# Optimization experiments

Hardware: AMD Instinct MI355X
Metric: run time of the kernel (lower is better)

The kernel has to match this reference:

```python
import jax, jax.numpy as jnp
import numpy as np

HIDDEN = 256
HEADS = 8
HEAD_DIM = HIDDEN // HEADS
RBF_DIM = 50
EPS = 1e-5


def setup_inputs() -> dict:
    key = jax.random.key(0)
    ks = jax.random.split(key, 16)
    L, P = 1024, 2048
    s = 0.02
    inp = {
        "lig_h": jax.random.normal(ks[0], (L, HIDDEN), jnp.float32),
        "prot_h": jax.random.normal(ks[1], (P, HIDDEN), jnp.float32),
        "rbf": jax.random.uniform(ks[2], (L, P, RBF_DIM), jnp.float32),
        "L": L,
        "P": P,
        "Wq": jax.random.normal(ks[3], (HIDDEN, HIDDEN), jnp.float32) * s,
        "bq": jnp.zeros((HIDDEN,), jnp.float32),
        "Wk": jax.random.normal(ks[4], (HIDDEN, HIDDEN), jnp.float32) * s,
        "bk": jnp.zeros((HIDDEN,), jnp.float32),
        "Wv": jax.random.normal(ks[5], (HIDDEN, HIDDEN), jnp.float32) * s,
        "bv": jnp.zeros((HIDDEN,), jnp.float32),
        "Wrbf": jax.random.normal(ks[6], (RBF_DIM, HEADS), jnp.float32) * s,
        "brbf": jnp.zeros((HEADS,), jnp.float32),
        "Wo": jax.random.normal(ks[7], (HIDDEN, HIDDEN), jnp.float32) * s,
        "bo": jnp.zeros((HIDDEN,), jnp.float32),
        "gamma": jnp.ones((HIDDEN,), jnp.float32),
        "beta": jnp.zeros((HIDDEN,), jnp.float32),
    }
    return inp


def reference(lig_h, prot_h, rbf, L, P, Wq, bq, Wk, bk, Wv, bv, Wrbf, brbf, Wo, bo, gamma, beta):
    scale = float(HEAD_DIM) ** 0.5
    Q = (lig_h @ Wq + bq).reshape(L, HEADS, HEAD_DIM)
    K = (prot_h @ Wk + bk).reshape(P, HEADS, HEAD_DIM)
    V = (prot_h @ Wv + bv).reshape(P, HEADS, HEAD_DIM)
    attn = jnp.einsum('lhd,phd->lph', Q, K) / scale
    dist_bias = rbf @ Wrbf + brbf          # [L, P, H]
    attn = attn + dist_bias
    attn_weights = jax.nn.softmax(attn, axis=1)  # over P (protein) axis
    attended = jnp.einsum('lph,phd->lhd', attn_weights, V).reshape(L, HIDDEN)
    y = lig_h + attended @ Wo + bo
    mu = jnp.mean(y, axis=-1, keepdims=True)
    var = jnp.var(y, axis=-1, keepdims=True)
    lig_h_out = (y - mu) * jax.lax.rsqrt(var + EPS) * gamma + beta
    return (lig_h_out, attn_weights)
```

## Files before the change

kernel.cpp:

```cpp
#include <hip/hip_runtime.h>
#include <hip/hip_bf16.h>

#define L_SZ 1024
#define P_SZ 2048
#define HID 256
#define NH 8
#define HD 32
#define NRBF 50
#define CH 32
#define NCH 64

typedef unsigned int uint32;
typedef _Float16 half2_t __attribute__((ext_vector_type(2)));
typedef __fp16 fp16x2_t __attribute__((ext_vector_type(2)));

__constant__ float kINV_SCALE = 0.17677669529663687f;

static __device__ __forceinline__ unsigned short f2h(float f) {
    union { _Float16 h; unsigned short u; } x; x.h = (_Float16)f; return x.u;
}
static __device__ __forceinline__ float h2f(unsigned short u) {
    union { unsigned short u; _Float16 h; } x; x.u = u; return (float)x.h;
}
static __device__ __forceinline__ half2_t u2h2(uint32 u) {
    union { uint32 u; half2_t h; } x; x.u = u; return x.h;
}
static __device__ __forceinline__ half2_t pk2h(float a, float b) {
    union { fp16x2_t p; half2_t h; } x; x.p = __builtin_amdgcn_cvt_pkrtz(a, b); return x.h;
}

static __device__ __forceinline__ void g2l16(const void* g, void* l) {
    __builtin_amdgcn_global_load_lds(
        (__attribute__((address_space(1))) void*)(void*)g,
        (__attribute__((address_space(3))) void*)l, 16, 0, 0);
}
static __device__ __forceinline__ void g2l4(const void* g, void* l) {
    __builtin_amdgcn_global_load_lds(
        (__attribute__((address_space(1))) void*)(void*)g,
        (__attribute__((address_space(3))) void*)l, 4, 0, 0);
}

__global__ __launch_bounds__(64) void k_proj(
    const float* __restrict__ lig, const float* __restrict__ prot,
    const float* __restrict__ Wq, const float* __restrict__ bq,
    const float* __restrict__ Wk, const float* __restrict__ bk,
    const float* __restrict__ Wv, const float* __restrict__ bv,
    float* __restrict__ Qf, unsigned short* __restrict__ Kb,
    unsigned short* __restrict__ Vb)
{
    __shared__ float As[8 * HID];
    const int t = threadIdx.x;
    const int r0 = blockIdx.x * 8;

    const float* src; const float* W; const float* bias; int mode; int row0;
    if (r0 < L_SZ)            { src = lig  + (size_t)r0 * HID;               W = Wq; bias = bq; mode = 0; row0 = r0; }
    else if (r0 < L_SZ + P_SZ){ src = prot + (size_t)(r0 - L_SZ) * HID;      W = Wk; bias = bk; mode = 1; row0 = r0 - L_SZ; }
    else                      { src = prot + (size_t)(r0 - L_SZ - P_SZ)*HID; W = Wv; bias = bv; mode = 2; row0 = r0 - L_SZ - P_SZ; }

    float4* A4 = (float4*)As;
    const float4* S4 = (const float4*)src;
    #pragma unroll
    for (int j = 0; j < 8; ++j) A4[t + j * 64] = S4[t + j * 64];
    __syncthreads();

    float acc[8][4];
    #pragma unroll
    for (int r = 0; r < 8; ++r)
        #pragma unroll
        for (int c = 0; c < 4; ++c) acc[r][c] = 0.f;

    for (int k4 = 0; k4 < 64; ++k4) {
        float4 av[8];
        #pragma unroll
        for (int r = 0; r < 8; ++r) av[r] = A4[r * 64 + k4];
        #pragma unroll
        for (int kk = 0; kk < 4; ++kk) {
            const float* wr = W + (size_t)(k4 * 4 + kk) * HID + t;
            #pragma unroll
            for (int c = 0; c < 4; ++c) {
                float wv = wr[c * 64];
                #pragma unroll
                for (int r = 0; r < 8; ++r)
                    acc[r][c] += ((const float*)&av[r])[kk] * wv;
            }
        }
    }

    #pragma unroll
    for (int c = 0; c < 4; ++c) {
        const int col = t + c * 64;
        const float bb = bias[col];
        #pragma unroll
        for (int r = 0; r < 8; ++r) {
            float v = acc[r][c] + bb;
            size_t idx = (size_t)(row0 + r) * HID + col;
            if (mode == 0)      Qf[idx] = v;
            else if (mode == 1) Kb[idx] = f2h(v);
            else                Vb[idx] = f2h(v);
        }
    }
}

__global__ __launch_bounds__(256, 2) void k_attn(
    const float* __restrict__ rbf, const float* __restrict__ Qf,
    const unsigned short* __restrict__ Kb, const unsigned short* __restrict__ Vb,
    const float* __restrict__ Wrbf, const float* __restrict__ brbf,
    float* __restrict__ attn_out, float* __restrict__ att_ws)
{
    __shared__ __align__(16) char sm[78400];
    char* slgB = sm + 45568;
    float* red = (float*)(sm + 78336);

    const int t = threadIdx.x;
    const int lane = t & 63;
    const int wv = t >> 6;
    const int r = t & 31;
    const int h = t >> 5;
    const int l = blockIdx.x;

    auto stageKV = [&](const unsigned short* src, int c, char* dst) {
        const char* gb = (const char*)src + (size_t)c * (CH * 512);
        #pragma unroll
        for (int k = 0; k < 4; ++k) {
            int s = wv * 4 + k;
            int row = s * 2 + (lane >> 5);
            int off = ((lane & 31) ^ (row & 31)) << 4;
            g2l16(gb + row * 512 + off, dst + s * 1024);
        }
    };
    auto stageRBF = [&](int c, char* dst) {
        const char* gb = (const char*)rbf + (size_t)l * 409600 + (size_t)c * 6400;
        g2l16(gb + wv * 1024 + (lane << 4), dst + wv * 1024);
        if (wv == 0)      g2l16(gb + 4096 + (lane << 4), dst + 4096);
        else if (wv == 1) g2l16(gb + 5120 + (lane << 4), dst + 5120);
        else if (wv == 2) g2l4 (gb + 6144 + (lane << 2), dst + 6144);
    };

    half2_t wrb[25];
    #pragma unroll
    for (int j = 0; j < 25; ++j)
        wrb[j] = pk2h(Wrbf[(2 * j) * NH + h], Wrbf[(2 * j + 1) * NH + h]);
    const float bh = brbf[h];

    half2_t qp[16];
    {
        const float* qq = Qf + (size_t)l * HID + h * HD;
        #pragma unroll
        for (int n = 0; n < 16; ++n)
            qp[n] = pk2h(qq[2 * n], qq[2 * n + 1]);
    }

    const int doff = ((((h >> 1) ^ ((r >> 3) & 3)) << 2) | ((h & 1) << 1));

    stageKV(Kb, 0, sm);
    stageRBF(0, sm + 32768);
    asm volatile("s_waitcnt vmcnt(0)" ::: "memory");
    __syncthreads();

    float mx = -3.0e38f;
    for (int c = 0; c < NCH; ++c) {
        const int cb = c & 1;
        char* kb = sm + cb * 16384;
        char* rb = sm + 32768 + cb * 6400;
        if (c + 1 < NCH) {
            stageKV(Kb, c + 1, sm + (cb ^ 1) * 16384);
            stageRBF(c + 1, sm + 32768 + (cb ^ 1) * 6400);
        }
        float bias = bh;
        const char* rrow = rb + r * 200;
        #pragma unroll
        for (int j = 0; j < 25; ++j) {
            float2 v = *(const float2*)(rrow + j * 8);
            bias = __builtin_amdgcn_fdot2(pk2h(v.x, v.y), wrb[j], bias, false);
        }
        float qk = 0.f;
        const char* krow = kb + r * 512;
        #pragma unroll
        for (int jw = 0; jw < 4; ++jw) {
            int off = (h * 64 + jw * 16) ^ (r << 4);
            uint4 kk = *(const uint4*)(krow + off);
            qk = __builtin_amdgcn_fdot2(u2h2(kk.x), qp[jw * 4 + 0], qk, false);
            qk = __builtin_amdgcn_fdot2(u2h2(kk.y), qp[jw * 4 + 1], qk, false);
            qk = __builtin_amdgcn_fdot2(u2h2(kk.z), qp[jw * 4 + 2], qk, false);
            qk = __builtin_amdgcn_fdot2(u2h2(kk.w), qp[jw * 4 + 3], qk, false);
        }
        float lg = qk * kINV_SCALE + bias;
        mx = fmaxf(mx, lg);
        *(unsigned short*)(slgB + (size_t)((c * CH + r) * 16) + doff) = f2h(lg);

        asm volatile("s_waitcnt vmcnt(0)" ::: "memory");
        __syncthreads();
    }

    #pragma unroll
    for (int msk = 1; msk <= 16; msk <<= 1) mx = fmaxf(mx, __shfl_xor(mx, msk));
    float sme = 0.f;
    for (int c = 0; c < NCH; ++c) {
        unsigned short u = *(const unsigned short*)(slgB + (size_t)((c * CH + r) * 16) + doff);
        sme += __expf(h2f(u) - mx);
    }
    #pragma unroll
    for (int msk = 1; msk <= 16; msk <<= 1) sme += __shfl_xor(sme, msk);
    if ((t & 31) == 0) { red[h * 2] = mx; red[h * 2 + 1] = 1.f / sme; }

    stageKV(Vb, 0, sm);
    __syncthreads();

    {
        float mh[8], ih[8];
        #pragma unroll
        for (int hh = 0; hh < 8; ++hh) { mh[hh] = red[hh * 2]; ih[hh] = red[hh * 2 + 1]; }
        const int sel = t & 1;
        float m0 = sel ? mh[4] : mh[0], i0 = sel ? ih[4] : ih[0];
        float m1 = sel ? mh[5] : mh[1], i1 = sel ? ih[5] : ih[1];
        float m2 = sel ? mh[6] : mh[2], i2 = sel ? ih[6] : ih[2];
        float m3 = sel ? mh[7] : mh[3], i3 = sel ? ih[7] : ih[3];
        const int x = (t >> 4) & 3;
        const int dA = (((2 * sel)     ^ x) << 2);
        const int dB = (((2 * sel + 1) ^ x) << 2);
        float4* ao = (float4*)(attn_out + (size_t)l * (P_SZ * NH));
        #pragma unroll
        for (int n = 0; n < 16; ++n) {
            int f = t + n * 256;
            int p = (t >> 1) + n * 128;
            char* rowp = slgB + p * 16;
            uint32 a = *(uint32*)(rowp + dA);
            uint32 b = *(uint32*)(rowp + dB);
            float w0 = __expf(h2f((unsigned short)(a & 0xffffu)) - m0) * i0;
            float w1 = __expf(h2f((unsigned short)(a >> 16))     - m1) * i1;
            float w2 = __expf(h2f((unsigned short)(b & 0xffffu)) - m2) * i2;
            float w3 = __expf(h2f((unsigned short)(b >> 16))     - m3) * i3;
            ao[f] = make_float4(w0, w1, w2, w3);
            *(uint32*)(rowp + dA) = (uint32)f2h(w0) | ((uint32)f2h(w1) << 16);
            *(uint32*)(rowp + dB) = (uint32)f2h(w2) | ((uint32)f2h(w3) << 16);
        }
    }
    asm volatile("s_waitcnt vmcnt(0)" ::: "memory");
    __syncthreads();

    {
        const int h3 = t >> 5;
        const int dq = (t >> 3) & 3;
        const int ps = t & 7;
        const int vinner = h3 * 64 + dq * 16;
        float acc[8] = {0.f, 0.f, 0.f, 0.f, 0.f, 0.f, 0.f, 0.f};
        for (int c = 0; c < NCH; ++c) {
            const int cb = c & 1;
            char* vb = sm + cb * 16384;
            if (c + 1 < NCH) stageKV(Vb, c + 1, sm + (cb ^ 1) * 16384);
            #pragma unroll
            for (int m = 0; m < 4; ++m) {
                int rr = m * 8 + ps;
                int p = c * CH + rr;
                int dw = (((h3 >> 1) ^ m) << 2) | ((h3 & 1) << 1);
                float w = h2f(*(const unsigned short*)(slgB + p * 16 + dw));
                int off = vinner ^ (rr << 4);
                uint4 vvv = *(const uint4*)(vb + rr * 512 + off);
                half2_t x0 = u2h2(vvv.x), x1 = u2h2(vvv.y), x2 = u2h2(vvv.z), x3 = u2h2(vvv.w);
                acc[0] += w * (float)x0.x; acc[1] += w * (float)x0.y;
                acc[2] += w * (float)x1.x; acc[3] += w * (float)x1.y;
                acc[4] += w * (float)x2.x; acc[5] += w * (float)x2.y;
                acc[6] += w * (float)x3.x; acc[7] += w * (float)x3.y;
            }
            asm volatile("s_waitcnt vmcnt(0)" ::: "memory");
            __syncthreads();
        }
        #pragma unroll
        for (int d = 0; d < 8; ++d) {
            acc[d] += __shfl_xor(acc[d], 1);
            acc[d] += __shfl_xor(acc[d], 2);
            acc[d] += __shfl_xor(acc[d], 4);
        }
        if (ps == 0) {
            float* dst = att_ws + (size_t)l * HID + h3 * HD + dq * 8;
            *(float4*)dst       = make_float4(acc[0], acc[1], acc[2], acc[3]);
            *(float4*)(dst + 4) = make_float4(acc[4], acc[5], acc[6], acc[7]);
        }
    }
}

__global__ __launch_bounds__(256) void k_out(
    const float* __restrict__ att, const float* __restrict__ lig,
    const float* __restrict__ Wo, const float* __restrict__ bo,
    const float* __restrict__ gamma, const float* __restrict__ beta,
    float* __restrict__ out)
{
    __shared__ float a[HID];
    __shared__ float red[8];
    const int l = blockIdx.x, t = threadIdx.x;
    if (t < 64) ((float4*)a)[t] = ((const float4*)(att + (size_t)l * HID))[t];
    __syncthreads();

    float acc = bo[t];
    for (int k4 = 0; k4 < 64; ++k4) {
        float4 av = ((float4*)a)[k4];
        const float* wr = Wo + (size_t)(k4 * 4) * HID + t;
        acc += av.x * wr[0];
        acc += av.y * wr[HID];
        acc += av.z * wr[2 * HID];
        acc += av.w * wr[3 * HID];
    }
    float y = lig[(size_t)l * HID + t] + acc;

    float s = y, sq = y * y;
    #pragma unroll
    for (int msk = 1; msk < 64; msk <<= 1) {
        s  += __shfl_xor(s, msk);
        sq += __shfl_xor(sq, msk);
    }
    const int lane = t & 63, wvi = t >> 6;
    if (lane == 0) { red[wvi * 2] = s; red[wvi * 2 + 1] = sq; }
    __syncthreads();
    float ts = red[0] + red[2] + red[4] + red[6];
    float tq = red[1] + red[3] + red[5] + red[7];
    float mu = ts * (1.0f / HID);
    float var = tq * (1.0f / HID) - mu * mu;
    out[(size_t)l * HID + t] = (y - mu) * rsqrtf(var + 1e-5f) * gamma[t] + beta[t];
}

extern "C" void kernel_launch(void* const* d_in, const int* in_sizes, int n_in,
                              void* d_out, int out_size, void* d_ws, size_t ws_size,
                              hipStream_t stream)
{
    (void)in_sizes; (void)n_in; (void)out_size; (void)ws_size;

    const float* lig   = (const float*)d_in[0];
    const float* prot  = (const float*)d_in[1];
    const float* rbf   = (const float*)d_in[2];
    const float* Wq    = (const float*)d_in[5];
    const float* bq    = (const float*)d_in[6];
    const float* Wk    = (const float*)d_in[7];
    const float* bk    = (const float*)d_in[8];
    const float* Wv    = (const float*)d_in[9];
    const float* bv    = (const float*)d_in[10];
    const float* Wrbf  = (const float*)d_in[11];
    const float* brbf  = (const float*)d_in[12];
    const float* Wo    = (const float*)d_in[13];
    const float* bo    = (const float*)d_in[14];
    const float* gamma = (const float*)d_in[15];
    const float* beta  = (const float*)d_in[16];

    float* out0 = (float*)d_out;
    float* attn = (float*)d_out + (size_t)L_SZ * HID;

    char* ws = (char*)d_ws;
    float*          Qf     = (float*)ws;
    unsigned short* Kb     = (unsigned short*)(ws + (1u << 20));
    unsigned short* Vb     = (unsigned short*)(ws + (2u << 20));
    float*          att_ws = (float*)(ws + (3u << 20));

    hipLaunchKernelGGL(k_proj, dim3((L_SZ + 2 * P_SZ) / 8), dim3(64), 0, stream,
                       lig, prot, Wq, bq, Wk, bk, Wv, bv, Qf, Kb, Vb);
    hipLaunchKernelGGL(k_attn, dim3(L_SZ), dim3(256), 0, stream,
                       rbf, Qf, Kb, Vb, Wrbf, brbf, attn, att_ws);
    hipLaunchKernelGGL(k_out, dim3(L_SZ), dim3(256), 0, stream,
                       att_ws, lig, Wo, bo, gamma, beta, out0);
}
```

Measured before the change: 314.4 us.

## Keep logits in global attn output instead of LDS; online softmax stats

```diff
diff --git a/kernel.cpp b/kernel.cpp
--- a/kernel.cpp
+++ b/kernel.cpp
@@ -18,9 +18,6 @@
 
 static __device__ __forceinline__ unsigned short f2h(float f) {
     union { _Float16 h; unsigned short u; } x; x.h = (_Float16)f; return x.u;
-}
-static __device__ __forceinline__ float h2f(unsigned short u) {
-    union { unsigned short u; _Float16 h; } x; x.u = u; return (float)x.h;
 }
 static __device__ __forceinline__ half2_t u2h2(uint32 u) {
     union { uint32 u; half2_t h; } x; x.u = u; return x.h;
@@ -101,15 +98,14 @@
     }
 }
 
-__global__ __launch_bounds__(256, 2) void k_attn(
+__global__ __launch_bounds__(256, 3) void k_attn(
     const float* __restrict__ rbf, const float* __restrict__ Qf,
     const unsigned short* __restrict__ Kb, const unsigned short* __restrict__ Vb,
     const float* __restrict__ Wrbf, const float* __restrict__ brbf,
     float* __restrict__ attn_out, float* __restrict__ att_ws)
 {
-    __shared__ __align__(16) char sm[78400];
-    char* slgB = sm + 45568;
-    float* red = (float*)(sm + 78336);
+    __shared__ __align__(16) char sm[45632];
+    float* red = (float*)(sm + 45568);
 
     const int t = threadIdx.x;
     const int lane = t & 63;
@@ -117,6 +113,7 @@
     const int r = t & 31;
     const int h = t >> 5;
     const int l = blockIdx.x;
+    float* aoL = attn_out + (size_t)l * (P_SZ * NH);
 
     auto stageKV = [&](const unsigned short* src, int c, char* dst) {
         const char* gb = (const char*)src + (size_t)c * (CH * 512);
@@ -150,14 +147,12 @@
             qp[n] = pk2h(qq[2 * n], qq[2 * n + 1]);
     }
 
-    const int doff = ((((h >> 1) ^ ((r >> 3) & 3)) << 2) | ((h & 1) << 1));
-
     stageKV(Kb, 0, sm);
     stageRBF(0, sm + 32768);
     asm volatile("s_waitcnt vmcnt(0)" ::: "memory");
     __syncthreads();
 
-    float mx = -3.0e38f;
+    float mx = -3.0e38f, sme = 0.f;
     for (int c = 0; c < NCH; ++c) {
         const int cb = c & 1;
         char* kb = sm + cb * 16384;
@@ -185,54 +180,37 @@
             qk = __builtin_amdgcn_fdot2(u2h2(kk.w), qp[jw * 4 + 3], qk, false);
         }
         float lg = qk * kINV_SCALE + bias;
-        mx = fmaxf(mx, lg);
-        *(unsigned short*)(slgB + (size_t)((c * CH + r) * 16) + doff) = f2h(lg);
+        float nm = fmaxf(mx, lg);
+        sme = sme * __expf(mx - nm) + __expf(lg - nm);
+        mx = nm;
+        aoL[(c * CH + r) * NH + h] = lg;
 
         asm volatile("s_waitcnt vmcnt(0)" ::: "memory");
         __syncthreads();
     }
 
     #pragma unroll
-    for (int msk = 1; msk <= 16; msk <<= 1) mx = fmaxf(mx, __shfl_xor(mx, msk));
-    float sme = 0.f;
-    for (int c = 0; c < NCH; ++c) {
-        unsigned short u = *(const unsigned short*)(slgB + (size_t)((c * CH + r) * 16) + doff);
-        sme += __expf(h2f(u) - mx);
-    }
-    #pragma unroll
-    for (int msk = 1; msk <= 16; msk <<= 1) sme += __shfl_xor(sme, msk);
+    for (int msk = 1; msk <= 16; msk <<= 1) {
+        float om = __shfl_xor(mx, msk);
+        float os = __shfl_xor(sme, msk);
+        float nm = fmaxf(mx, om);
+        sme = sme * __expf(mx - nm) + os * __expf(om - nm);
+        mx = nm;
+    }
     if ((t & 31) == 0) { red[h * 2] = mx; red[h * 2 + 1] = 1.f / sme; }
 
     stageKV(Vb, 0, sm);
     __syncthreads();
 
     {
-        float mh[8], ih[8];
-        #pragma unroll
-        for (int hh = 0; hh < 8; ++hh) { mh[hh] = red[hh * 2]; ih[hh] = red[hh * 2 + 1]; }
-        const int sel = t & 1;
-        float m0 = sel ? mh[4] : mh[0], i0 = sel ? ih[4] : ih[0];
-        float m1 = sel ? mh[5] : mh[1], i1 = sel ? ih[5] : ih[1];
-        float m2 = sel ? mh[6] : mh[2], i2 = sel ? ih[6] : ih[2];
-        float m3 = sel ? mh[7] : mh[3], i3 = sel ? ih[7] : ih[3];
-        const int x = (t >> 4) & 3;
-        const int dA = (((2 * sel)     ^ x) << 2);
-        const int dB = (((2 * sel + 1) ^ x) << 2);
-        float4* ao = (float4*)(attn_out + (size_t)l * (P_SZ * NH));
-        #pragma unroll
-        for (int n = 0; n < 16; ++n) {
+        const int h2 = t & 7;
+        const float m = red[h2 * 2];
+        const float inv = red[h2 * 2 + 1];
+        #pragma unroll 4
+        for (int n = 0; n < 64; ++n) {
             int f = t + n * 256;
-            int p = (t >> 1) + n * 128;
-            char* rowp = slgB + p * 16;
-            uint32 a = *(uint32*)(rowp + dA);
-            uint32 b = *(uint32*)(rowp + dB);
-            float w0 = __expf(h2f((unsigned short)(a & 0xffffu)) - m0) * i0;
-            float w1 = __expf(h2f((unsigned short)(a >> 16))     - m1) * i1;
-            float w2 = __expf(h2f((unsigned short)(b & 0xffffu)) - m2) * i2;
-            float w3 = __expf(h2f((unsigned short)(b >> 16))     - m3) * i3;
-            ao[f] = make_float4(w0, w1, w2, w3);
-            *(uint32*)(rowp + dA) = (uint32)f2h(w0) | ((uint32)f2h(w1) << 16);
-            *(uint32*)(rowp + dB) = (uint32)f2h(w2) | ((uint32)f2h(w3) << 16);
+            float w = __expf(aoL[f] - m) * inv;
+            aoL[f] = w;
         }
     }
     asm volatile("s_waitcnt vmcnt(0)" ::: "memory");
@@ -251,9 +229,7 @@
             #pragma unroll
             for (int m = 0; m < 4; ++m) {
                 int rr = m * 8 + ps;
-                int p = c * CH + rr;
-                int dw = (((h3 >> 1) ^ m) << 2) | ((h3 & 1) << 1);
-                float w = h2f(*(const unsigned short*)(slgB + p * 16 + dw));
+                float w = aoL[(c * CH + rr) * NH + h3];
                 int off = vinner ^ (rr << 4);
                 uint4 vvv = *(const uint4*)(vb + rr * 512 + off);
                 half2_t x0 = u2h2(vvv.x), x1 = u2h2(vvv.y), x2 = u2h2(vvv.z), x3 = u2h2(vvv.w);
```

After: 390.7 us. +24.3%, slower.
